# Kernel optimization log

Hardware: AMD Instinct MI355X
Metric: run time of the kernel (lower is better)

Reference implementation:

```python
import jax, jax.numpy as jnp
import numpy as np

B, S_IMG, S_TXT = 1, 2048, 512
H, D = 24, 128
DIM = H * D
EPS = 1e-6


def _rmsnorm(x, g):
    # per-head RMSNorm over last dim (head_dim), computed in fp32 like torch RMSNorm
    xf = x.astype(jnp.float32)
    var = jnp.mean(jnp.square(xf), axis=-1, keepdims=True)
    return (xf * jax.lax.rsqrt(var + EPS)).astype(x.dtype) * g


def _rope(x, cos, sin):
    # x: [b,h,s,d]; pairs are consecutive (view_as_complex of reshape(...,-1,2))
    xr, xi = x[..., ::2], x[..., 1::2]
    o_r = xr * cos - xi * sin
    o_i = xr * sin + xi * cos
    return jnp.stack([o_r, o_i], axis=-1).reshape(x.shape).astype(x.dtype)


def _heads(x):  # [b,s,(h d)] -> [b,h,s,d]
    b, s, _ = x.shape
    return x.reshape(b, s, H, D).transpose(0, 2, 1, 3)


def setup_inputs() -> dict:
    key = jax.random.key(0)
    ks = jax.random.split(key, 12)

    def lin(k):
        return (jax.random.normal(k, (DIM, DIM), jnp.float32) * 0.02,
                jnp.zeros((DIM,), jnp.float32))

    image = jax.random.normal(ks[0], (B, S_IMG, DIM), jnp.float32)
    text = jax.random.normal(ks[1], (B, S_TXT, DIM), jnp.float32)
    inv = 1.0 / (10000.0 ** (np.arange(0, D, 2, dtype=np.float32) / D))
    ang_i = np.arange(S_IMG, dtype=np.float32)[:, None] * inv[None, :]
    ang_t = np.arange(S_TXT, dtype=np.float32)[:, None] * inv[None, :]
    Wq, bq = lin(ks[2]); Wk, bk = lin(ks[3]); Wv, bv = lin(ks[4])
    Waq, baq = lin(ks[5]); Wak, bak = lin(ks[6]); Wav, bav = lin(ks[7])
    Wo, bo = lin(ks[8]); Wao, bao = lin(ks[9])
    return {
        'image': image, 'text': text,
        'img_cos': jnp.asarray(np.cos(ang_i)), 'img_sin': jnp.asarray(np.sin(ang_i)),
        'txt_cos': jnp.asarray(np.cos(ang_t)), 'txt_sin': jnp.asarray(np.sin(ang_t)),
        'Wq': Wq, 'bq': bq, 'Wk': Wk, 'bk': bk, 'Wv': Wv, 'bv': bv,
        'Waq': Waq, 'baq': baq, 'Wak': Wak, 'bak': bak, 'Wav': Wav, 'bav': bav,
        'gq': jnp.ones((D,), jnp.float32), 'gk': jnp.ones((D,), jnp.float32),
        'gaq': jnp.ones((D,), jnp.float32), 'gak': jnp.ones((D,), jnp.float32),
        'Wo': Wo, 'bo': bo, 'Wao': Wao, 'bao': bao,
    }


def reference(image, text, img_cos, img_sin, txt_cos, txt_sin,
              Wq, bq, Wk, bk, Wv, bv, Waq, baq, Wak, bak, Wav, bav,
              gq, gk, gaq, gak, Wo, bo, Wao, bao):
    img_q = _heads(image @ Wq + bq)
    img_k = _heads(image @ Wk + bk)
    img_v = _heads(image @ Wv + bv)
    txt_q = _heads(text @ Waq + baq)
    txt_k = _heads(text @ Wak + bak)
    txt_v = _heads(text @ Wav + bav)

    img_q = _rope(_rmsnorm(img_q, gq), img_cos, img_sin)
    img_k = _rope(_rmsnorm(img_k, gk), img_cos, img_sin)
    txt_q = _rope(_rmsnorm(txt_q, gaq), txt_cos, txt_sin)
    txt_k = _rope(_rmsnorm(txt_k, gak), txt_cos, txt_sin)

    q = jnp.concatenate([txt_q, img_q], axis=2)  # text first
    k = jnp.concatenate([txt_k, img_k], axis=2)
    v = jnp.concatenate([txt_v, img_v], axis=2)

    scale = float(D) ** -0.5
    scores = jnp.einsum('bhqd,bhkd->bhqk', q, k) * scale
    probs = jax.nn.softmax(scores, axis=-1)
    attn = jnp.einsum('bhqk,bhkd->bhqd', probs, v)
    b, _, s, _ = attn.shape
    joint = attn.transpose(0, 2, 1, 3).reshape(b, s, DIM)

    txt_out = joint[:, :S_TXT, :] @ Wao + bao
    img_out = joint[:, S_TXT:, :] @ Wo + bo
    return img_out, txt_out
```

## Files before the change

kernel.cpp:

```cpp
#include <hip/hip_runtime.h>
#include <stdint.h>

typedef uint32_t u32;
typedef float f32x4 __attribute__((ext_vector_type(4)));
typedef u32 u32x4 __attribute__((ext_vector_type(4)));
typedef short s16x8 __attribute__((ext_vector_type(8)));

#define DI __device__ __forceinline__

DI unsigned short f2bf(float f) {
    u32 u = __builtin_bit_cast(u32, f);
    u32 r = (u + 0x7fffu + ((u >> 16) & 1u)) >> 16;
    return (unsigned short)r;
}
DI float bf2f(unsigned short s) {
    u32 u = ((u32)s) << 16;
    return __builtin_bit_cast(float, u);
}
DI u32 pack2(unsigned short lo, unsigned short hi) { return (u32)lo | ((u32)hi << 16); }

DI void mfma_bf16(f32x4& acc, u32x4 a, u32x4 b) {
    acc = __builtin_amdgcn_mfma_f32_16x16x32_bf16(
        __builtin_bit_cast(s16x8, a), __builtin_bit_cast(s16x8, b), acc, 0, 0, 0);
}

DI void gload16(const unsigned short* g, unsigned short* l) {
    __builtin_amdgcn_global_load_lds(
        (const __attribute__((address_space(1))) uint32_t*)(uintptr_t)g,
        (__attribute__((address_space(3))) uint32_t*)(uint32_t)(uintptr_t)l, 16, 0, 0);
}

__global__ __launch_bounds__(256) void k_cast(const float* __restrict__ X,
                                              unsigned short* __restrict__ Y, int n4) {
    int i = blockIdx.x * 256 + threadIdx.x;
    if (i < n4) {
        float4 v = ((const float4*)X)[i];
        ushort4 o;
        o.x = f2bf(v.x); o.y = f2bf(v.y); o.z = f2bf(v.z); o.w = f2bf(v.w);
        ((ushort4*)Y)[i] = o;
    }
}

__global__ __launch_bounds__(256) void k_tcast(const float* __restrict__ W,
                                               unsigned short* __restrict__ Wt) {
    __shared__ float t[64][65];
    const int K = 3072;
    int k0 = blockIdx.y * 64, n0 = blockIdx.x * 64;
    int tid = threadIdx.x;
    int r = tid >> 4, c4 = (tid & 15) * 4;
#pragma unroll
    for (int i = 0; i < 4; i++) {
        float4 v = *(const float4*)(W + (size_t)(k0 + r + i * 16) * K + n0 + c4);
        t[r + i * 16][c4 + 0] = v.x;
        t[r + i * 16][c4 + 1] = v.y;
        t[r + i * 16][c4 + 2] = v.z;
        t[r + i * 16][c4 + 3] = v.w;
    }
    __syncthreads();
#pragma unroll
    for (int i = 0; i < 4; i++) {
        int n = r + i * 16;
        ushort4 o;
        o.x = f2bf(t[c4 + 0][n]);
        o.y = f2bf(t[c4 + 1][n]);
        o.z = f2bf(t[c4 + 2][n]);
        o.w = f2bf(t[c4 + 3][n]);
        *(ushort4*)(Wt + (size_t)(n0 + n) * K + k0 + c4) = o;
    }
}

__global__ __launch_bounds__(256) void k_gemm(
    const unsigned short* __restrict__ Atxt, const unsigned short* __restrict__ Aimg,
    const unsigned short* __restrict__ Bt0, const unsigned short* __restrict__ Bt1,
    const float* __restrict__ bias0, const float* __restrict__ bias1,
    void* out0, void* out1, int epi) {
    __shared__ unsigned short Al[2][4096];
    __shared__ unsigned short Bl[2][4096];
    const int K = 3072;
    int tid = threadIdx.x;
    int lane = tid & 63, w = tid >> 6;
    int wr = w >> 1, wc = w & 1;
    int l15 = lane & 15, lg = lane >> 4;
    int m0 = blockIdx.y * 128, n0 = blockIdx.x * 128;
    int sel = (int)(m0 >= 512);
    const unsigned short* Bt = sel ? Bt1 : Bt0;
    const float* bias = sel ? bias1 : bias0;
    const unsigned short* Abase =
        sel ? (Aimg + (size_t)(m0 - 512) * K) : (Atxt + (size_t)m0 * K);

    f32x4 acc[4][4] = {};

    int srow = w * 32 + (lane >> 2);
    int colsw = ((lane & 3) ^ ((lane >> 3) & 3)) * 8;
    const unsigned short* Ag = Abase + (size_t)srow * K + colsw;
    const unsigned short* Bg = Bt + (size_t)(n0 + srow) * K + colsw;
    int gsw = (l15 >> 1) & 3;

#pragma unroll
    for (int i = 0; i < 2; i++) {
        gload16(Ag + (size_t)i * 16 * K, &Al[0][w * 1024 + i * 512]);
        gload16(Bg + (size_t)i * 16 * K, &Bl[0][w * 1024 + i * 512]);
    }
    __syncthreads();

    int cur = 0;
    for (int k0 = 0; k0 < K; k0 += 32) {
        if (k0 + 32 < K) {
#pragma unroll
            for (int i = 0; i < 2; i++) {
                gload16(Ag + (size_t)i * 16 * K + k0 + 32, &Al[cur ^ 1][w * 1024 + i * 512]);
                gload16(Bg + (size_t)i * 16 * K + k0 + 32, &Bl[cur ^ 1][w * 1024 + i * 512]);
            }
        }
        u32x4 af[4], bf[4];
#pragma unroll
        for (int i = 0; i < 4; i++) {
            int ar = wr * 64 + i * 16 + l15;
            int br = wc * 64 + i * 16 + l15;
            af[i] = *(const u32x4*)&Al[cur][ar * 32 + (lg ^ gsw) * 8];
            bf[i] = *(const u32x4*)&Bl[cur][br * 32 + (lg ^ gsw) * 8];
        }
#pragma unroll
        for (int i = 0; i < 4; i++)
#pragma unroll
            for (int j = 0; j < 4; j++) mfma_bf16(acc[i][j], af[i], bf[j]);
        __syncthreads();
        cur ^= 1;
    }

#pragma unroll
    for (int j = 0; j < 4; j++) {
        int n = n0 + wc * 64 + j * 16 + l15;
        float b = bias[n];
        int h = n >> 7, d = n & 127;
#pragma unroll
        for (int i = 0; i < 4; i++) {
            if (epi == 1) {
                int sb = m0 + wr * 64 + (i >> 1) * 32 + lg * 8 + (i & 1) * 4;
                ushort4 o;
                o.x = f2bf(acc[i][j][0] + b);
                o.y = f2bf(acc[i][j][1] + b);
                o.z = f2bf(acc[i][j][2] + b);
                o.w = f2bf(acc[i][j][3] + b);
                *(ushort4*)((unsigned short*)out0 + ((size_t)h * 128 + d) * 2560 + sb) = o;
            } else {
#pragma unroll
                for (int r = 0; r < 4; r++) {
                    int s = m0 + wr * 64 + i * 16 + lg * 4 + r;
                    float v = acc[i][j][r] + b;
                    if (epi == 2) {
                        float* ob = (s < 512) ? (float*)out0 + (size_t)s * 3072
                                              : (float*)out1 + (size_t)(s - 512) * 3072;
                        ob[n] = v;
                    } else {
                        ((unsigned short*)out0)[((size_t)h * 2560 + s) * 128 + d] = f2bf(v);
                    }
                }
            }
        }
    }
}

__global__ __launch_bounds__(256) void k_normrope(unsigned short* __restrict__ Q,
                                                  unsigned short* __restrict__ Kb,
                                                  const float* gq, const float* gk,
                                                  const float* gaq, const float* gak,
                                                  const float* img_cos, const float* img_sin,
                                                  const float* txt_cos, const float* txt_sin) {
    int w = threadIdx.x >> 6, lane = threadIdx.x & 63;
    int s = blockIdx.x * 4 + w;
    int h = blockIdx.y;
    int tensor = blockIdx.z;
    unsigned short* base = (tensor ? Kb : Q) + ((size_t)h * 2560 + s) * 128;
    bool txt = s < 512;
    const float* g = tensor ? (txt ? gak : gk) : (txt ? gaq : gq);
    const float* ct = txt ? txt_cos + (size_t)s * 64 : img_cos + (size_t)(s - 512) * 64;
    const float* st = txt ? txt_sin + (size_t)s * 64 : img_sin + (size_t)(s - 512) * 64;

    u32 v = ((u32*)base)[lane];
    float xr = bf2f((unsigned short)(v & 0xffff));
    float xi = bf2f((unsigned short)(v >> 16));
    float ss = xr * xr + xi * xi;
#pragma unroll
    for (int m = 1; m < 64; m <<= 1) ss += __shfl_xor(ss, m);
    float rs = rsqrtf(ss * (1.0f / 128.0f) + 1e-6f);
    float c = ct[lane], sn = st[lane];
    float g0 = g[2 * lane], g1 = g[2 * lane + 1];
    xr *= rs * g0;
    xi *= rs * g1;
    float orr = xr * c - xi * sn;
    float oi = xr * sn + xi * c;
    ((u32*)base)[lane] = pack2(f2bf(orr), f2bf(oi));
}

__global__ __launch_bounds__(128) void k_attn(const unsigned short* __restrict__ Q,
                                              const unsigned short* __restrict__ Kb,
                                              const unsigned short* __restrict__ Vt,
                                              unsigned short* __restrict__ J) {
    __shared__ unsigned short Kl[64 * 128];
    __shared__ unsigned short Vl[128 * 64];
    int tid = threadIdx.x;
    int lane = tid & 63, w = tid >> 6;
    int l15 = lane & 15, lg = lane >> 4;
    int h = blockIdx.y, qb = blockIdx.x;
    int q0 = qb * 32 + w * 16;
    const float scale = 0.08838834764831845f;

    u32x4 qf[4];
    const unsigned short* qrow = Q + ((size_t)h * 2560 + q0 + l15) * 128;
#pragma unroll
    for (int c = 0; c < 4; c++) qf[c] = *(const u32x4*)(qrow + c * 32 + lg * 8);

    float m_run = -1e30f, l_run = 0.0f;
    f32x4 oa[8] = {};

    int tr = tid >> 4, tg16 = tid & 15;
    const unsigned short* Kg = Kb + (size_t)h * 2560 * 128;
    const unsigned short* Vg = Vt + ((size_t)h * 128 + tid) * 2560;
    int dsw = l15 & 7;

    for (int kt = 0; kt < 40; kt++) {
        __syncthreads();
#pragma unroll
        for (int i = 0; i < 8; i++) {
            int row = tr + i * 8;
            ((u32x4*)Kl)[row * 16 + (tg16 ^ (row & 7))] =
                *(const u32x4*)(Kg + (size_t)(kt * 64 + row) * 128 + tg16 * 8);
        }
#pragma unroll
        for (int g = 0; g < 8; g++)
            ((u32x4*)Vl)[tid * 8 + (g ^ (tid & 7))] = *(const u32x4*)(Vg + kt * 64 + g * 8);
        __syncthreads();

        f32x4 sc[4] = {};
#pragma unroll
        for (int ks = 0; ks < 4; ks++)
#pragma unroll
            for (int c = 0; c < 4; c++) {
                int row = ks * 16 + l15;
                u32x4 kf = ((const u32x4*)Kl)[row * 16 + ((4 * c + lg) ^ dsw)];
                mfma_bf16(sc[ks], kf, qf[c]);
            }

        float ps[16];
        float tmax = -1e30f;
#pragma unroll
        for (int ks = 0; ks < 4; ks++)
#pragma unroll
            for (int r = 0; r < 4; r++) {
                float sv = sc[ks][r] * scale;
                ps[ks * 4 + r] = sv;
                tmax = fmaxf(tmax, sv);
            }
        tmax = fmaxf(tmax, __shfl_xor(tmax, 16));
        tmax = fmaxf(tmax, __shfl_xor(tmax, 32));
        float m_new = fmaxf(m_run, tmax);
        float fsc = __expf(m_run - m_new);
        float lsum = 0.0f;
#pragma unroll
        for (int t = 0; t < 16; t++) {
            ps[t] = __expf(ps[t] - m_new);
            lsum += ps[t];
        }
        lsum += __shfl_xor(lsum, 16);
        lsum += __shfl_xor(lsum, 32);
        l_run = l_run * fsc + lsum;
        m_run = m_new;
#pragma unroll
        for (int dg = 0; dg < 8; dg++) oa[dg] *= fsc;

        u32x4 pb[2];
#pragma unroll
        for (int c = 0; c < 2; c++)
#pragma unroll
            for (int i = 0; i < 4; i++)
                pb[c][i] = pack2(f2bf(ps[8 * c + 2 * i]), f2bf(ps[8 * c + 2 * i + 1]));

#pragma unroll
        for (int dg = 0; dg < 8; dg++) {
            int d = dg * 16 + l15;
#pragma unroll
            for (int c = 0; c < 2; c++) {
                u32x4 vf = ((const u32x4*)Vl)[d * 8 + ((4 * c + lg) ^ dsw)];
                mfma_bf16(oa[dg], vf, pb[c]);
            }
        }
    }

    float inv = 1.0f / l_run;
#pragma unroll
    for (int dg = 0; dg < 8; dg++)
#pragma unroll
        for (int r = 0; r < 4; r++) {
            int d = dg * 16 + lg * 4 + r;
            J[(size_t)(q0 + l15) * 3072 + h * 128 + d] = f2bf(oa[dg][r] * inv);
        }
}

extern "C" void kernel_launch(void* const* d_in, const int* in_sizes, int n_in,
                              void* d_out, int out_size, void* d_ws, size_t ws_size,
                              hipStream_t stream) {
    const float* image = (const float*)d_in[0];
    const float* text = (const float*)d_in[1];
    const float* img_cos = (const float*)d_in[2];
    const float* img_sin = (const float*)d_in[3];
    const float* txt_cos = (const float*)d_in[4];
    const float* txt_sin = (const float*)d_in[5];
    const float* Wq = (const float*)d_in[6];
    const float* bq = (const float*)d_in[7];
    const float* Wk = (const float*)d_in[8];
    const float* bk = (const float*)d_in[9];
    const float* Wv = (const float*)d_in[10];
    const float* bv = (const float*)d_in[11];
    const float* Waq = (const float*)d_in[12];
    const float* baq = (const float*)d_in[13];
    const float* Wak = (const float*)d_in[14];
    const float* bak = (const float*)d_in[15];
    const float* Wav = (const float*)d_in[16];
    const float* bav = (const float*)d_in[17];
    const float* gq = (const float*)d_in[18];
    const float* gk = (const float*)d_in[19];
    const float* gaq = (const float*)d_in[20];
    const float* gak = (const float*)d_in[21];
    const float* Wo = (const float*)d_in[22];
    const float* bo = (const float*)d_in[23];
    const float* Wao = (const float*)d_in[24];
    const float* bao = (const float*)d_in[25];

    char* A = (char*)d_ws;
    char* B = (char*)d_out;
    unsigned short* WT0 = (unsigned short*)A;
    unsigned short* WT1 = (unsigned short*)(A + 18874368);
    unsigned short* Qb = (unsigned short*)(A + 37748736);
    unsigned short* Kbuf = (unsigned short*)(A + 53477376);
    unsigned short* J = WT0;
    unsigned short* WTao = WT1;
    unsigned short* WTo = Qb;
    unsigned short* XI = (unsigned short*)B;
    unsigned short* XT = (unsigned short*)(B + 12582912);
    unsigned short* VT = (unsigned short*)(B + 15728640);
    float* out_img = (float*)d_out;
    float* out_txt = (float*)d_out + 6291456;

    dim3 tg(48, 48);
    dim3 gj(24, 20, 1);

    k_cast<<<6144, 256, 0, stream>>>(image, XI, 1572864);
    k_cast<<<1536, 256, 0, stream>>>(text, XT, 393216);

    k_tcast<<<tg, 256, 0, stream>>>(Waq, WT0);
    k_tcast<<<tg, 256, 0, stream>>>(Wq, WT1);
    k_gemm<<<gj, 256, 0, stream>>>(XT, XI, WT0, WT1, baq, bq, Qb, Qb, 0);

    k_tcast<<<tg, 256, 0, stream>>>(Wak, WT0);
    k_tcast<<<tg, 256, 0, stream>>>(Wk, WT1);
    k_gemm<<<gj, 256, 0, stream>>>(XT, XI, WT0, WT1, bak, bk, Kbuf, Kbuf, 0);

    k_tcast<<<tg, 256, 0, stream>>>(Wav, WT0);
    k_tcast<<<tg, 256, 0, stream>>>(Wv, WT1);
    k_gemm<<<gj, 256, 0, stream>>>(XT, XI, WT0, WT1, bav, bv, VT, VT, 1);

    k_normrope<<<dim3(640, 24, 2), 256, 0, stream>>>(Qb, Kbuf, gq, gk, gaq, gak,
                                                     img_cos, img_sin, txt_cos, txt_sin);

    k_attn<<<dim3(80, 24), 128, 0, stream>>>(Qb, Kbuf, VT, J);

    k_tcast<<<tg, 256, 0, stream>>>(Wao, WTao);
    k_tcast<<<tg, 256, 0, stream>>>(Wo, WTo);
    k_gemm<<<gj, 256, 0, stream>>>(J, J + (size_t)512 * 3072, WTao, WTo, bao, bo,
                                   out_txt, out_img, 2);
}
```

Measured before the change: 983.9 us.

## Double the attention block to four waves and prefetch next K/V tile into registers

The attention kernel now runs 256 threads per block covering 64 query rows, which halves the number of times each K/V tile is loaded into LDS per query. The next K/V tile is prefetched into registers while the current tile is computed, so global-load latency can overlap with the MFMA work. s_setprio is raised around the MFMA sections. The cost is higher register pressure from the prefetch buffers and half as many blocks (960) in the grid.

```diff
diff --git a/kernel.cpp b/kernel.cpp
--- a/kernel.cpp
+++ b/kernel.cpp
@@ -193,7 +193,7 @@
     ((u32*)base)[lane] = pack2(f2bf(orr), f2bf(oi));
 }
 
-__global__ __launch_bounds__(128) void k_attn(const unsigned short* __restrict__ Q,
+__global__ __launch_bounds__(256) void k_attn(const unsigned short* __restrict__ Q,
                                               const unsigned short* __restrict__ Kb,
                                               const unsigned short* __restrict__ Vt,
                                               unsigned short* __restrict__ J) {
@@ -203,7 +203,7 @@
     int lane = tid & 63, w = tid >> 6;
     int l15 = lane & 15, lg = lane >> 4;
     int h = blockIdx.y, qb = blockIdx.x;
-    int q0 = qb * 32 + w * 16;
+    int q0 = qb * 64 + w * 16;
     const float scale = 0.08838834764831845f;
 
     u32x4 qf[4];
@@ -215,24 +215,42 @@
     f32x4 oa[8] = {};
 
     int tr = tid >> 4, tg16 = tid & 15;
+    int vd = tid >> 1, vh = tid & 1;
     const unsigned short* Kg = Kb + (size_t)h * 2560 * 128;
-    const unsigned short* Vg = Vt + ((size_t)h * 128 + tid) * 2560;
+    const unsigned short* Vg = Vt + ((size_t)h * 128 + vd) * 2560;
     int dsw = l15 & 7;
+
+    u32x4 kreg[4], vreg[4];
+#pragma unroll
+    for (int i = 0; i < 4; i++)
+        kreg[i] = *(const u32x4*)(Kg + (size_t)(tr + i * 16) * 128 + tg16 * 8);
+#pragma unroll
+    for (int j = 0; j < 4; j++)
+        vreg[j] = *(const u32x4*)(Vg + (vh * 4 + j) * 8);
 
     for (int kt = 0; kt < 40; kt++) {
         __syncthreads();
 #pragma unroll
-        for (int i = 0; i < 8; i++) {
-            int row = tr + i * 8;
-            ((u32x4*)Kl)[row * 16 + (tg16 ^ (row & 7))] =
-                *(const u32x4*)(Kg + (size_t)(kt * 64 + row) * 128 + tg16 * 8);
-        }
-#pragma unroll
-        for (int g = 0; g < 8; g++)
-            ((u32x4*)Vl)[tid * 8 + (g ^ (tid & 7))] = *(const u32x4*)(Vg + kt * 64 + g * 8);
+        for (int i = 0; i < 4; i++) {
+            int row = tr + i * 16;
+            ((u32x4*)Kl)[row * 16 + (tg16 ^ (row & 7))] = kreg[i];
+        }
+#pragma unroll
+        for (int j = 0; j < 4; j++)
+            ((u32x4*)Vl)[vd * 8 + ((vh * 4 + j) ^ (vd & 7))] = vreg[j];
+        if (kt + 1 < 40) {
+#pragma unroll
+            for (int i = 0; i < 4; i++)
+                kreg[i] = *(const u32x4*)(Kg + (size_t)((kt + 1) * 64 + tr + i * 16) * 128 +
+                                          tg16 * 8);
+#pragma unroll
+            for (int j = 0; j < 4; j++)
+                vreg[j] = *(const u32x4*)(Vg + (kt + 1) * 64 + (vh * 4 + j) * 8);
+        }
         __syncthreads();
 
         f32x4 sc[4] = {};
+        __builtin_amdgcn_s_setprio(1);
 #pragma unroll
         for (int ks = 0; ks < 4; ks++)
 #pragma unroll
@@ -241,6 +259,7 @@
                 u32x4 kf = ((const u32x4*)Kl)[row * 16 + ((4 * c + lg) ^ dsw)];
                 mfma_bf16(sc[ks], kf, qf[c]);
             }
+        __builtin_amdgcn_s_setprio(0);
 
         float ps[16];
         float tmax = -1e30f;
@@ -276,6 +295,7 @@
             for (int i = 0; i < 4; i++)
                 pb[c][i] = pack2(f2bf(ps[8 * c + 2 * i]), f2bf(ps[8 * c + 2 * i + 1]));
 
+        __builtin_amdgcn_s_setprio(1);
 #pragma unroll
         for (int dg = 0; dg < 8; dg++) {
             int d = dg * 16 + l15;
@@ -285,6 +305,7 @@
                 mfma_bf16(oa[dg], vf, pb[c]);
             }
         }
+        __builtin_amdgcn_s_setprio(0);
     }
 
     float inv = 1.0f / l_run;
@@ -363,7 +384,7 @@
     k_normrope<<<dim3(640, 24, 2), 256, 0, stream>>>(Qb, Kbuf, gq, gk, gaq, gak,
                                                      img_cos, img_sin, txt_cos, txt_sin);
 
-    k_attn<<<dim3(80, 24), 128, 0, stream>>>(Qb, Kbuf, VT, J);
+    k_attn<<<dim3(40, 24), 256, 0, stream>>>(Qb, Kbuf, VT, J);
 
     k_tcast<<<tg, 256, 0, stream>>>(Wao, WTao);
     k_tcast<<<tg, 256, 0, stream>>>(Wo, WTo);
```

Measured after the change: 791.9 us. 19.5% less time.
